# Optimization experiments

Hardware: AMD Instinct MI355X
Metric: run time of the kernel (lower is better)

## Reference

```python
import jax, jax.numpy as jnp
import numpy as np

TOKENS, IN_F, OUT_F = 8192, 4096, 16384


def setup_inputs() -> dict:
    key = jax.random.key(0)
    k1, k2, k3, k4 = jax.random.split(key, 4)
    input = jax.random.normal(k1, (TOKENS, IN_F), dtype=jnp.float32)
    # int8 quantized weight, stored [out_features, in_features] like the torch buffer
    weight = jax.random.randint(k2, (OUT_F, IN_F), -127, 128, dtype=jnp.int8)
    # per-output-channel dequant scale
    weight_scale = jax.random.uniform(k3, (OUT_F,), dtype=jnp.float32, minval=0.001, maxval=0.02)
    bias = jax.random.normal(k4, (OUT_F,), dtype=jnp.float32) * 0.01
    return {"input": input, "weight": weight, "weight_scale": weight_scale, "bias": bias}


def reference(input, weight, weight_scale, bias):
    # Fallback path of DynamicQuantizeMatMul: dequantize B = weight.T * scale, then matmul.
    # B: [in_features, out_features]; scale broadcasts over out_features (columns).
    B = weight.astype(jnp.float32).T * weight_scale
    out = input @ B + bias  # [tokens, out_features]
    return out
```

## Files before the change

### kernel.cpp

```cpp
#include <hip/hip_runtime.h>

#define MDIM 8192
#define NDIM 16384
#define KDIM 4096

typedef int i32x4 __attribute__((ext_vector_type(4)));
typedef int i32x16 __attribute__((ext_vector_type(16)));
typedef float f32x4 __attribute__((ext_vector_type(4)));

__device__ __forceinline__ unsigned short f2bf(float f) {
  __bf16 h = (__bf16)f;
  return __builtin_bit_cast(unsigned short, h);
}

__device__ __forceinline__ void gload_lds16(const void* g, void* l) {
  __builtin_amdgcn_global_load_lds(
      (const __attribute__((address_space(1))) unsigned int*)g,
      (__attribute__((address_space(3))) unsigned int*)l, 16, 0, 0);
}


__global__ __launch_bounds__(256) void cvt_a_q8(const float* __restrict__ a,
                                                signed char* __restrict__ o,
                                                float* __restrict__ sA) {
  const int row = blockIdx.x;
  const int tid = threadIdx.x;
  float v[16];
  const float4* s4 = (const float4*)(a + (long long)row * KDIM + tid * 16);
#pragma unroll
  for (int i = 0; i < 4; ++i) {
    float4 f = s4[i];
    v[i * 4 + 0] = f.x; v[i * 4 + 1] = f.y;
    v[i * 4 + 2] = f.z; v[i * 4 + 3] = f.w;
  }
  float m = 0.f;
#pragma unroll
  for (int i = 0; i < 16; ++i) m = fmaxf(m, fabsf(v[i]));
#pragma unroll
  for (int off = 32; off; off >>= 1) m = fmaxf(m, __shfl_xor(m, off));
  __shared__ float red[4];
  if ((tid & 63) == 0) red[tid >> 6] = m;
  __syncthreads();
  m = fmaxf(fmaxf(red[0], red[1]), fmaxf(red[2], red[3]));
  const float inv = m > 0.f ? 127.f / m : 0.f;
  if (tid == 0) sA[row] = m * (1.f / 127.f);
  union { signed char c[16]; uint4 u; } p;
#pragma unroll
  for (int i = 0; i < 16; ++i)
    p.c[i] = (signed char)__float2int_rn(v[i] * inv);
  const int kt = tid >> 2, ks = tid & 3;
  *(uint4*)(o + ((((long long)(row >> 8) * 64 + kt) * 4 + ks) << 12) +
            ((row & 255) << 4)) = p.u;
}

__global__ __launch_bounds__(256) void cvt_w_q8(const int* __restrict__ w,
                                                signed char* __restrict__ o) {
  const int nt = blockIdx.x >> 6;
  const int kt = blockIdx.x & 63;
  const int t = threadIdx.x;
  const int* src = w + (long long)(nt * 256 + t) * KDIM + kt * 64;
  signed char* dst = o + (((long long)(nt * 64 + kt) * 4) << 12) + (t << 4);
#pragma unroll
  for (int ks = 0; ks < 4; ++ks) {
    union { signed char c[16]; uint4 u; } p;
#pragma unroll
    for (int i = 0; i < 4; ++i) {
      int4 x = *(const int4*)(src + ks * 16 + i * 4);
      p.c[i * 4 + 0] = (signed char)x.x; p.c[i * 4 + 1] = (signed char)x.y;
      p.c[i * 4 + 2] = (signed char)x.z; p.c[i * 4 + 3] = (signed char)x.w;
    }
    *(uint4*)(dst + (ks << 12)) = p.u;
  }
}

__global__ __launch_bounds__(512, 2) void gemm_i8_v13(
    const signed char* __restrict__ Ab, const signed char* __restrict__ Wb,
    const float* __restrict__ sA, const float* __restrict__ sc,
    const float* __restrict__ bi, float* __restrict__ out) {
  __shared__ alignas(16) char sm[3 * 32768];
  const int tid = threadIdx.x;
  const int lane = tid & 63;
  const int wv = tid >> 6;
  const int l31 = lane & 31;
  const int l32 = lane >> 5;
  const int wr = wv >> 2;
  const int wc = wv & 3;
  const int c = blockIdx.x & 7;
  const int l = blockIdx.x >> 3;
  const int mA = ((c & 3) << 3) + (l & 7);
  const int nT = ((c >> 2) << 5) + (l >> 3);
  const int bm = mA << 8;
  const int bn = nT << 8;

  int aO[2][4], bO[2][2];
#pragma unroll
  for (int kk = 0; kk < 2; ++kk) {
#pragma unroll
    for (int mb = 0; mb < 4; ++mb)
      aO[kk][mb] = (kk * 2 + l32) * 4096 + (wr * 128 + mb * 32 + l31) * 16;
#pragma unroll
    for (int nb = 0; nb < 2; ++nb)
      bO[kk][nb] = 16384 + (kk * 2 + l32) * 4096 + (wc * 64 + nb * 32 + l31) * 16;
  }

  i32x16 acc[4][2] = {};

  const signed char* aSrc = Ab + ((long long)mA << 20) + (tid << 4);
  const signed char* bSrc = Wb + ((long long)nT << 20) + (tid << 4);
  const int t16 = tid << 4;

  char* bR = &sm[0];
  char* bN = &sm[32768];
  char* bS = &sm[65536];

  auto STAGE = [&](char* slot) {
    gload_lds16(aSrc, slot + t16);
    gload_lds16(aSrc + 8192, slot + 8192 + t16);
    gload_lds16(bSrc, slot + 16384 + t16);
    gload_lds16(bSrc + 8192, slot + 24576 + t16);
    aSrc += 16384;
    bSrc += 16384;
  };

  STAGE(bR);
  STAGE(bN);
  asm volatile("s_waitcnt vmcnt(4)" ::: "memory");
  __builtin_amdgcn_s_barrier();

  for (int t = 0; t < 64; ++t) {
    if (t <= 61) STAGE(bS);
    __builtin_amdgcn_s_setprio(1);
    i32x4 aF[2][4], bF[2][2];
#pragma unroll
    for (int kk = 0; kk < 2; ++kk) {
#pragma unroll
      for (int mb = 0; mb < 4; ++mb) aF[kk][mb] = *(const i32x4*)(bR + aO[kk][mb]);
#pragma unroll
      for (int nb = 0; nb < 2; ++nb) bF[kk][nb] = *(const i32x4*)(bR + bO[kk][nb]);
    }
#pragma unroll
    for (int kk = 0; kk < 2; ++kk)
#pragma unroll
      for (int mb = 0; mb < 4; ++mb)
#pragma unroll
        for (int nb = 0; nb < 2; ++nb)
          acc[mb][nb] = __builtin_amdgcn_mfma_i32_32x32x32_i8(
              aF[kk][mb], bF[kk][nb], acc[mb][nb], 0, 0, 0);
    __builtin_amdgcn_s_setprio(0);
    if (t <= 61) {
      asm volatile("s_waitcnt vmcnt(4)" ::: "memory");
    } else if (t == 62) {
      asm volatile("s_waitcnt vmcnt(0)" ::: "memory");
    }
    if (t < 63) __builtin_amdgcn_s_barrier();
    char* tmp = bR; bR = bN; bN = bS; bS = tmp;
  }

  float sv[2], bv[2];
#pragma unroll
  for (int nb = 0; nb < 2; ++nb) {
    const int cc = bn + wc * 64 + nb * 32 + l31;
    sv[nb] = sc[cc];
    bv[nb] = bi[cc];
  }
#pragma unroll
  for (int mb = 0; mb < 4; ++mb) {
    const int rb = bm + wr * 128 + mb * 32 + l32 * 4;
    float sa[16];
#pragma unroll
    for (int r = 0; r < 16; ++r) sa[r] = sA[rb + (r & 3) + 8 * (r >> 2)];
#pragma unroll
    for (int nb = 0; nb < 2; ++nb) {
      const int cc = bn + wc * 64 + nb * 32 + l31;
#pragma unroll
      for (int r = 0; r < 16; ++r) {
        const long long row = rb + (r & 3) + 8 * (r >> 2);
        __builtin_nontemporal_store(
            (float)acc[mb][nb][r] * (sa[r] * sv[nb]) + bv[nb],
            out + row * NDIM + cc);
      }
    }
  }
}

__global__ __launch_bounds__(256, 2) void gemm_inline(
    const float* __restrict__ A, const int* __restrict__ W,
    const float* __restrict__ sc, const float* __restrict__ bi,
    float* __restrict__ out) {
  typedef __bf16 bf16x8 __attribute__((ext_vector_type(8)));
  __shared__ unsigned short As[128 * 72];
  __shared__ unsigned short Bs[128 * 72];
  const int tid = threadIdx.x;
  const int lane = tid & 63;
  const int wv = tid >> 6;
  const int wg = (blockIdx.x & 7) * 1024 + (blockIdx.x >> 3);
  const int bm = (wg & 63) * 128;
  const int bn = (wg >> 6) * 128;
  const int wr = (wv >> 1) * 64;
  const int wc = (wv & 1) * 64;
  const int r16 = lane & 15;
  const int g4 = lane >> 4;

  f32x4 acc[4][4] = {};

  const int srow = tid >> 4;
  const int sc4 = (tid & 15) << 2;
  const float* aPtr = A + (long long)(bm + srow) * KDIM + sc4;
  const int* wPtr = W + (long long)(bn + srow) * KDIM + sc4;

  for (int kt = 0; kt < KDIM; kt += 64) {
    float4 av[8];
    int4 wv4[8];
#pragma unroll
    for (int j = 0; j < 8; ++j)
      av[j] = *(const float4*)(aPtr + (long long)j * 16 * KDIM + kt);
#pragma unroll
    for (int j = 0; j < 8; ++j)
      wv4[j] = *(const int4*)(wPtr + (long long)j * 16 * KDIM + kt);
    __syncthreads();
#pragma unroll
    for (int j = 0; j < 8; ++j) {
      ushort4 u;
      u.x = f2bf(av[j].x); u.y = f2bf(av[j].y);
      u.z = f2bf(av[j].z); u.w = f2bf(av[j].w);
      *(ushort4*)&As[(srow + j * 16) * 72 + sc4] = u;
    }
#pragma unroll
    for (int j = 0; j < 8; ++j) {
      ushort4 u;
      u.x = f2bf((float)wv4[j].x); u.y = f2bf((float)wv4[j].y);
      u.z = f2bf((float)wv4[j].z); u.w = f2bf((float)wv4[j].w);
      *(ushort4*)&Bs[(srow + j * 16) * 72 + sc4] = u;
    }
    __syncthreads();
#pragma unroll
    for (int ks = 0; ks < 2; ++ks) {
      bf16x8 aF[4], bF[4];
      const int kofs = ks * 32 + g4 * 8;
#pragma unroll
      for (int m2 = 0; m2 < 4; ++m2)
        aF[m2] = *(const bf16x8*)&As[(wr + m2 * 16 + r16) * 72 + kofs];
#pragma unroll
      for (int n2 = 0; n2 < 4; ++n2)
        bF[n2] = *(const bf16x8*)&Bs[(wc + n2 * 16 + r16) * 72 + kofs];
#pragma unroll
      for (int m2 = 0; m2 < 4; ++m2)
#pragma unroll
        for (int n2 = 0; n2 < 4; ++n2)
          acc[m2][n2] = __builtin_amdgcn_mfma_f32_16x16x32_bf16(
              aF[m2], bF[n2], acc[m2][n2], 0, 0, 0);
    }
  }

  float sv[4], bv[4];
#pragma unroll
  for (int n2 = 0; n2 < 4; ++n2) {
    const int c = bn + wc + n2 * 16 + r16;
    sv[n2] = sc[c];
    bv[n2] = bi[c];
  }
#pragma unroll
  for (int m2 = 0; m2 < 4; ++m2) {
    const int row0 = bm + wr + m2 * 16 + g4 * 4;
#pragma unroll
    for (int n2 = 0; n2 < 4; ++n2) {
      const int c = bn + wc + n2 * 16 + r16;
      float* op = out + (long long)row0 * NDIM + c;
#pragma unroll
      for (int r = 0; r < 4; ++r)
        op[(long long)r * NDIM] = acc[m2][n2][r] * sv[n2] + bv[n2];
    }
  }
}

extern "C" void kernel_launch(void* const* d_in, const int* in_sizes, int n_in,
                              void* d_out, int out_size, void* d_ws, size_t ws_size,
                              hipStream_t stream) {
  const float* A = (const float*)d_in[0];
  const int* W = (const int*)d_in[1];
  const float* sc = (const float*)d_in[2];
  const float* bi = (const float*)d_in[3];
  float* out = (float*)d_out;

  const size_t needA = (size_t)MDIM * KDIM;
  const size_t needW = (size_t)NDIM * KDIM;
  const size_t offS = needA + needW;
  const size_t need = offS + (size_t)MDIM * 4;

  if (d_ws != nullptr && ws_size >= need) {
    signed char* Ab = (signed char*)d_ws;
    signed char* Wb = (signed char*)d_ws + needA;
    float* sA = (float*)((char*)d_ws + offS);
    cvt_a_q8<<<8192, 256, 0, stream>>>(A, Ab, sA);
    cvt_w_q8<<<4096, 256, 0, stream>>>(W, Wb);
    gemm_i8_v13<<<2048, 512, 0, stream>>>(Ab, Wb, sA, sc, bi, out);
  } else {
    gemm_inline<<<8192, 256, 0, stream>>>(A, W, sc, bi, out);
  }
}
```

Before: 656.7 us.

## Switch GEMM main loop to 4-slot LDS ring with paired k-tiles per barrier

Grows the shared-memory staging ring from three to four 32KB slots. The main loop now loads two k-tiles into one slot pair while computing the other pair, then issues one full vmcnt(0) wait and one barrier per two tiles. The goal is to halve the barrier and wait overhead per k-step. In exchange it raises LDS use per block to 128KB and replaces the partial vmcnt(4) wait with a full drain each iteration, which can expose more load latency at pair boundaries.

```diff
diff --git a/kernel.cpp b/kernel.cpp
--- a/kernel.cpp
+++ b/kernel.cpp
@@ -73,11 +73,11 @@
   }
 }
 
-__global__ __launch_bounds__(512, 2) void gemm_i8_v13(
+__global__ __launch_bounds__(512, 2) void gemm_i8_v14(
     const signed char* __restrict__ Ab, const signed char* __restrict__ Wb,
     const float* __restrict__ sA, const float* __restrict__ sc,
     const float* __restrict__ bi, float* __restrict__ out) {
-  __shared__ alignas(16) char sm[3 * 32768];
+  __shared__ alignas(16) char sm[4 * 32768];
   const int tid = threadIdx.x;
   const int lane = tid & 63;
   const int wv = tid >> 6;
@@ -109,9 +109,10 @@
   const signed char* bSrc = Wb + ((long long)nT << 20) + (tid << 4);
   const int t16 = tid << 4;
 
-  char* bR = &sm[0];
-  char* bN = &sm[32768];
-  char* bS = &sm[65536];
+  char* const S0 = sm;
+  char* const S1 = sm + 32768;
+  char* const S2 = sm + 65536;
+  char* const S3 = sm + 98304;
 
   auto STAGE = [&](char* slot) {
     gload_lds16(aSrc, slot + t16);
@@ -122,22 +123,18 @@
     bSrc += 16384;
   };
 
-  STAGE(bR);
-  STAGE(bN);
-  asm volatile("s_waitcnt vmcnt(4)" ::: "memory");
-  __builtin_amdgcn_s_barrier();
-
-  for (int t = 0; t < 64; ++t) {
-    if (t <= 61) STAGE(bS);
+  auto TILE = [&](const char* slot) {
+    i32x4 aF[2][4], bF[2][2];
+#pragma unroll
+    for (int kk = 0; kk < 2; ++kk) {
+#pragma unroll
+      for (int mb = 0; mb < 4; ++mb)
+        aF[kk][mb] = *(const i32x4*)(slot + aO[kk][mb]);
+#pragma unroll
+      for (int nb = 0; nb < 2; ++nb)
+        bF[kk][nb] = *(const i32x4*)(slot + bO[kk][nb]);
+    }
     __builtin_amdgcn_s_setprio(1);
-    i32x4 aF[2][4], bF[2][2];
-#pragma unroll
-    for (int kk = 0; kk < 2; ++kk) {
-#pragma unroll
-      for (int mb = 0; mb < 4; ++mb) aF[kk][mb] = *(const i32x4*)(bR + aO[kk][mb]);
-#pragma unroll
-      for (int nb = 0; nb < 2; ++nb) bF[kk][nb] = *(const i32x4*)(bR + bO[kk][nb]);
-    }
 #pragma unroll
     for (int kk = 0; kk < 2; ++kk)
 #pragma unroll
@@ -147,14 +144,29 @@
           acc[mb][nb] = __builtin_amdgcn_mfma_i32_32x32x32_i8(
               aF[kk][mb], bF[kk][nb], acc[mb][nb], 0, 0, 0);
     __builtin_amdgcn_s_setprio(0);
-    if (t <= 61) {
-      asm volatile("s_waitcnt vmcnt(4)" ::: "memory");
-    } else if (t == 62) {
-      asm volatile("s_waitcnt vmcnt(0)" ::: "memory");
-    }
-    if (t < 63) __builtin_amdgcn_s_barrier();
-    char* tmp = bR; bR = bN; bN = bS; bS = tmp;
-  }
+  };
+
+  STAGE(S0);
+  STAGE(S1);
+  asm volatile("s_waitcnt vmcnt(0)" ::: "memory");
+  __builtin_amdgcn_s_barrier();
+
+#define PAIRF(sE, sO, tE, tO)                              \
+  STAGE(tE);                                               \
+  STAGE(tO);                                               \
+  TILE(sE);                                                \
+  TILE(sO);                                                \
+  asm volatile("s_waitcnt vmcnt(0)" ::: "memory");         \
+  __builtin_amdgcn_s_barrier();
+
+  for (int i = 0; i < 15; ++i) {
+    PAIRF(S0, S1, S2, S3)
+    PAIRF(S2, S3, S0, S1)
+  }
+  PAIRF(S0, S1, S2, S3)
+#undef PAIRF
+  TILE(S2);
+  TILE(S3);
 
   float sv[2], bv[2];
 #pragma unroll
@@ -293,7 +305,7 @@
     float* sA = (float*)((char*)d_ws + offS);
     cvt_a_q8<<<8192, 256, 0, stream>>>(A, Ab, sA);
     cvt_w_q8<<<4096, 256, 0, stream>>>(W, Wb);
-    gemm_i8_v13<<<2048, 512, 0, stream>>>(Ab, Wb, sA, sc, bi, out);
+    gemm_i8_v14<<<2048, 512, 0, stream>>>(Ab, Wb, sA, sc, bi, out);
   } else {
     gemm_inline<<<8192, 256, 0, stream>>>(A, W, sc, bi, out);
   }
```

New measurement: 645.1 us. No clear change (-1.8%).

## Load GEMM fragments directly from global into registers, dropping LDS staging

Applied to the files above, without the earlier changes.

Replaces the triple-buffered LDS pipeline (global_load_lds plus barriers) with direct global-to-register fragment loads, double-buffered in registers with software pipelining. This removes the LDS round trip and block barriers. In exchange, fragments are no longer shared across waves through LDS, so each wave re-reads data from L2/global and memory traffic rises. Launch bounds change to one block per CU, giving more registers but less occupancy.

```diff
diff --git a/kernel.cpp b/kernel.cpp
--- a/kernel.cpp
+++ b/kernel.cpp
@@ -11,12 +11,6 @@
 __device__ __forceinline__ unsigned short f2bf(float f) {
   __bf16 h = (__bf16)f;
   return __builtin_bit_cast(unsigned short, h);
-}
-
-__device__ __forceinline__ void gload_lds16(const void* g, void* l) {
-  __builtin_amdgcn_global_load_lds(
-      (const __attribute__((address_space(1))) unsigned int*)g,
-      (__attribute__((address_space(3))) unsigned int*)l, 16, 0, 0);
 }
 
 
@@ -73,11 +67,10 @@
   }
 }
 
-__global__ __launch_bounds__(512, 2) void gemm_i8_v13(
+__global__ __launch_bounds__(512, 1) void gemm_i8_v16(
     const signed char* __restrict__ Ab, const signed char* __restrict__ Wb,
     const float* __restrict__ sA, const float* __restrict__ sc,
     const float* __restrict__ bi, float* __restrict__ out) {
-  __shared__ alignas(16) char sm[3 * 32768];
   const int tid = threadIdx.x;
   const int lane = tid & 63;
   const int wv = tid >> 6;
@@ -92,52 +85,41 @@
   const int bm = mA << 8;
   const int bn = nT << 8;
 
-  int aO[2][4], bO[2][2];
+  const signed char* aP[2][4];
+  const signed char* bP[2][2];
 #pragma unroll
   for (int kk = 0; kk < 2; ++kk) {
 #pragma unroll
     for (int mb = 0; mb < 4; ++mb)
-      aO[kk][mb] = (kk * 2 + l32) * 4096 + (wr * 128 + mb * 32 + l31) * 16;
+      aP[kk][mb] = Ab + ((long long)mA << 20) + (kk * 2 + l32) * 4096 +
+                   (wr * 128 + mb * 32 + l31) * 16;
 #pragma unroll
     for (int nb = 0; nb < 2; ++nb)
-      bO[kk][nb] = 16384 + (kk * 2 + l32) * 4096 + (wc * 64 + nb * 32 + l31) * 16;
+      bP[kk][nb] = Wb + ((long long)nT << 20) + (kk * 2 + l32) * 4096 +
+                   (wc * 64 + nb * 32 + l31) * 16;
   }
 
   i32x16 acc[4][2] = {};
 
-  const signed char* aSrc = Ab + ((long long)mA << 20) + (tid << 4);
-  const signed char* bSrc = Wb + ((long long)nT << 20) + (tid << 4);
-  const int t16 = tid << 4;
-
-  char* bR = &sm[0];
-  char* bN = &sm[32768];
-  char* bS = &sm[65536];
-
-  auto STAGE = [&](char* slot) {
-    gload_lds16(aSrc, slot + t16);
-    gload_lds16(aSrc + 8192, slot + 8192 + t16);
-    gload_lds16(bSrc, slot + 16384 + t16);
-    gload_lds16(bSrc + 8192, slot + 24576 + t16);
-    aSrc += 16384;
-    bSrc += 16384;
+  auto LOADG = [&](i32x4 (&aF)[2][4], i32x4 (&bF)[2][2]) {
+#pragma unroll
+    for (int kk = 0; kk < 2; ++kk) {
+#pragma unroll
+      for (int mb = 0; mb < 4; ++mb) aF[kk][mb] = *(const i32x4*)aP[kk][mb];
+#pragma unroll
+      for (int nb = 0; nb < 2; ++nb) bF[kk][nb] = *(const i32x4*)bP[kk][nb];
+    }
   };
-
-  STAGE(bR);
-  STAGE(bN);
-  asm volatile("s_waitcnt vmcnt(4)" ::: "memory");
-  __builtin_amdgcn_s_barrier();
-
-  for (int t = 0; t < 64; ++t) {
-    if (t <= 61) STAGE(bS);
-    __builtin_amdgcn_s_setprio(1);
-    i32x4 aF[2][4], bF[2][2];
+  auto ADV = [&]() {
 #pragma unroll
     for (int kk = 0; kk < 2; ++kk) {
 #pragma unroll
-      for (int mb = 0; mb < 4; ++mb) aF[kk][mb] = *(const i32x4*)(bR + aO[kk][mb]);
-#pragma unroll
-      for (int nb = 0; nb < 2; ++nb) bF[kk][nb] = *(const i32x4*)(bR + bO[kk][nb]);
-    }
+      for (int mb = 0; mb < 4; ++mb) aP[kk][mb] += 16384;
+#pragma unroll
+      for (int nb = 0; nb < 2; ++nb) bP[kk][nb] += 16384;
+    }
+  };
+  auto MFMAS = [&](const i32x4 (&aF)[2][4], const i32x4 (&bF)[2][2]) {
 #pragma unroll
     for (int kk = 0; kk < 2; ++kk)
 #pragma unroll
@@ -146,15 +128,23 @@
         for (int nb = 0; nb < 2; ++nb)
           acc[mb][nb] = __builtin_amdgcn_mfma_i32_32x32x32_i8(
               aF[kk][mb], bF[kk][nb], acc[mb][nb], 0, 0, 0);
-    __builtin_amdgcn_s_setprio(0);
-    if (t <= 61) {
-      asm volatile("s_waitcnt vmcnt(4)" ::: "memory");
-    } else if (t == 62) {
-      asm volatile("s_waitcnt vmcnt(0)" ::: "memory");
-    }
-    if (t < 63) __builtin_amdgcn_s_barrier();
-    char* tmp = bR; bR = bN; bN = bS; bS = tmp;
-  }
+  };
+
+  i32x4 aFa[2][4], bFa[2][2], aFb[2][4], bFb[2][2];
+
+  LOADG(aFa, bFa);
+  ADV();
+  for (int i = 0; i < 31; ++i) {
+    LOADG(aFb, bFb);
+    ADV();
+    MFMAS(aFa, bFa);
+    LOADG(aFa, bFa);
+    ADV();
+    MFMAS(aFb, bFb);
+  }
+  LOADG(aFb, bFb);
+  MFMAS(aFa, bFa);
+  MFMAS(aFb, bFb);
 
   float sv[2], bv[2];
 #pragma unroll
@@ -293,7 +283,7 @@
     float* sA = (float*)((char*)d_ws + offS);
     cvt_a_q8<<<8192, 256, 0, stream>>>(A, Ab, sA);
     cvt_w_q8<<<4096, 256, 0, stream>>>(W, Wb);
-    gemm_i8_v13<<<2048, 512, 0, stream>>>(Ab, Wb, sA, sc, bi, out);
+    gemm_i8_v16<<<2048, 512, 0, stream>>>(Ab, Wb, sA, sc, bi, out);
   } else {
     gemm_inline<<<8192, 256, 0, stream>>>(A, W, sc, bi, out);
   }
```

Result: slower. 733.9 us (+11.7%).

## Load B fragments directly from global into double-buffered registers, bypassing LDS

Applied to the files above, without the earlier changes.

The weight tile is no longer staged through shared memory. Each wave loads its B MFMA fragments straight from global into registers one K-tile ahead, alternating two register buffers via an unrolled pair of tiles. LDS use halves and the wait counts are adjusted for the extra outstanding loads. The cost is duplicated global/L2 reads of B across waves, more VGPR pressure, and exposed global latency with only a single-tile prefetch.

```diff
diff --git a/kernel.cpp b/kernel.cpp
--- a/kernel.cpp
+++ b/kernel.cpp
@@ -73,11 +73,11 @@
   }
 }
 
-__global__ __launch_bounds__(512, 2) void gemm_i8_v13(
+__global__ __launch_bounds__(512, 2) void gemm_i8_v17(
     const signed char* __restrict__ Ab, const signed char* __restrict__ Wb,
     const float* __restrict__ sA, const float* __restrict__ sc,
     const float* __restrict__ bi, float* __restrict__ out) {
-  __shared__ alignas(16) char sm[3 * 32768];
+  __shared__ alignas(16) char sm[3 * 16384];
   const int tid = threadIdx.x;
   const int lane = tid & 63;
   const int wv = tid >> 6;
@@ -92,52 +92,63 @@
   const int bm = mA << 8;
   const int bn = nT << 8;
 
-  int aO[2][4], bO[2][2];
-#pragma unroll
-  for (int kk = 0; kk < 2; ++kk) {
+  int aO[2][4];
+#pragma unroll
+  for (int kk = 0; kk < 2; ++kk)
 #pragma unroll
     for (int mb = 0; mb < 4; ++mb)
       aO[kk][mb] = (kk * 2 + l32) * 4096 + (wr * 128 + mb * 32 + l31) * 16;
+
+  const signed char* bP[2][2];
+#pragma unroll
+  for (int kk = 0; kk < 2; ++kk)
 #pragma unroll
     for (int nb = 0; nb < 2; ++nb)
-      bO[kk][nb] = 16384 + (kk * 2 + l32) * 4096 + (wc * 64 + nb * 32 + l31) * 16;
-  }
+      bP[kk][nb] = Wb + ((long long)nT << 20) + (kk * 2 + l32) * 4096 +
+                   (wc * 64 + nb * 32 + l31) * 16;
 
   i32x16 acc[4][2] = {};
 
-  const signed char* aSrc = Ab + ((long long)mA << 20) + (tid << 4);
-  const signed char* bSrc = Wb + ((long long)nT << 20) + (tid << 4);
+  const signed char* aSt = Ab + ((long long)mA << 20) + (tid << 4);
   const int t16 = tid << 4;
 
   char* bR = &sm[0];
-  char* bN = &sm[32768];
-  char* bS = &sm[65536];
-
-  auto STAGE = [&](char* slot) {
-    gload_lds16(aSrc, slot + t16);
-    gload_lds16(aSrc + 8192, slot + 8192 + t16);
-    gload_lds16(bSrc, slot + 16384 + t16);
-    gload_lds16(bSrc + 8192, slot + 24576 + t16);
-    aSrc += 16384;
-    bSrc += 16384;
+  char* bN = &sm[16384];
+  char* bS = &sm[32768];
+
+  auto STAGE_A = [&](char* slot) {
+    gload_lds16(aSt, slot + t16);
+    gload_lds16(aSt + 8192, slot + 8192 + t16);
+    aSt += 16384;
   };
-
-  STAGE(bR);
-  STAGE(bN);
-  asm volatile("s_waitcnt vmcnt(4)" ::: "memory");
+  auto LOADB = [&](i32x4 (&bF)[2][2]) {
+#pragma unroll
+    for (int kk = 0; kk < 2; ++kk)
+#pragma unroll
+      for (int nb = 0; nb < 2; ++nb) {
+        bF[kk][nb] = *(const i32x4*)bP[kk][nb];
+        bP[kk][nb] += 16384;
+      }
+  };
+
+  i32x4 bFa[2][2], bFb[2][2];
+
+  STAGE_A(bR);
+  STAGE_A(bN);
+  LOADB(bFa);
+  asm volatile("s_waitcnt vmcnt(6)" ::: "memory");
   __builtin_amdgcn_s_barrier();
 
-  for (int t = 0; t < 64; ++t) {
-    if (t <= 61) STAGE(bS);
+  auto TILE = [&](int t, i32x4 (&bCur)[2][2], i32x4 (&bNxt)[2][2]) {
+    if (t <= 61) STAGE_A(bS);
+    if (t <= 62) LOADB(bNxt);
+    i32x4 aF[2][4];
+#pragma unroll
+    for (int kk = 0; kk < 2; ++kk)
+#pragma unroll
+      for (int mb = 0; mb < 4; ++mb)
+        aF[kk][mb] = *(const i32x4*)(bR + aO[kk][mb]);
     __builtin_amdgcn_s_setprio(1);
-    i32x4 aF[2][4], bF[2][2];
-#pragma unroll
-    for (int kk = 0; kk < 2; ++kk) {
-#pragma unroll
-      for (int mb = 0; mb < 4; ++mb) aF[kk][mb] = *(const i32x4*)(bR + aO[kk][mb]);
-#pragma unroll
-      for (int nb = 0; nb < 2; ++nb) bF[kk][nb] = *(const i32x4*)(bR + bO[kk][nb]);
-    }
 #pragma unroll
     for (int kk = 0; kk < 2; ++kk)
 #pragma unroll
@@ -145,15 +156,20 @@
 #pragma unroll
         for (int nb = 0; nb < 2; ++nb)
           acc[mb][nb] = __builtin_amdgcn_mfma_i32_32x32x32_i8(
-              aF[kk][mb], bF[kk][nb], acc[mb][nb], 0, 0, 0);
+              aF[kk][mb], bCur[kk][nb], acc[mb][nb], 0, 0, 0);
     __builtin_amdgcn_s_setprio(0);
     if (t <= 61) {
+      asm volatile("s_waitcnt vmcnt(6)" ::: "memory");
+    } else if (t == 62) {
       asm volatile("s_waitcnt vmcnt(4)" ::: "memory");
-    } else if (t == 62) {
-      asm volatile("s_waitcnt vmcnt(0)" ::: "memory");
     }
     if (t < 63) __builtin_amdgcn_s_barrier();
     char* tmp = bR; bR = bN; bN = bS; bS = tmp;
+  };
+
+  for (int i = 0; i < 32; ++i) {
+    TILE(2 * i, bFa, bFb);
+    TILE(2 * i + 1, bFb, bFa);
   }
 
   float sv[2], bv[2];
@@ -293,7 +309,7 @@
     float* sA = (float*)((char*)d_ws + offS);
     cvt_a_q8<<<8192, 256, 0, stream>>>(A, Ab, sA);
     cvt_w_q8<<<4096, 256, 0, stream>>>(W, Wb);
-    gemm_i8_v13<<<2048, 512, 0, stream>>>(Ab, Wb, sA, sc, bi, out);
+    gemm_i8_v17<<<2048, 512, 0, stream>>>(Ab, Wb, sA, sc, bi, out);
   } else {
     gemm_inline<<<8192, 256, 0, stream>>>(A, W, sc, bi, out);
   }
```

After: 692.5 us. 1.05x slower.
